# Optimization experiments

Measured on AMD Instinct MI355X. Metric: run time of the kernel, lower is better.

The kernel has to match this reference:

```python
import jax, jax.numpy as jnp
import numpy as np

# ---- config (mirrors the repo-level globals) ----
B, N = 8, 1024                 # batch, points per cloud
SHAPE_SIZE = 256               # per-point shape-code width
HEAD = 8                       # point_size + 1 - shape_size passthrough channels
SC_HID = 256                   # shape_code_encoder_hidden_dims = [256]
SC_OUT = 128                   # shape_code_encoder_output_size
E = 16                         # num_categories
INTER = HEAD + SC_OUT          # 136
ENC_DIMS = [INTER, 256, 512]   # encoder_hidden_dims
LATENT = 1024                  # latent_size
DEC_DIMS = [LATENT, 1024, 2048]
MAX_PTS, PSI = 1024, 7         # max_num_points, point_size_intermediate
DEC_OUT = (PSI + 1) * MAX_PTS  # 8192


def setup_inputs() -> dict:
    key = jax.random.key(0)
    ks = jax.random.split(key, 20)
    s = 0.02
    inp = {
        'x': jax.random.normal(ks[0], (B, HEAD + SHAPE_SIZE, N), jnp.float32),
        'cats': jax.random.randint(ks[1], (B, N), 0, E),
        # per-category shape encoders: Linear(256->256) ReLU Linear(256->128)
        'W1': jax.random.normal(ks[2], (E, SHAPE_SIZE, SC_HID), jnp.float32) * s,
        'b1': jnp.zeros((E, SC_HID), jnp.float32),
        'W2': jax.random.normal(ks[3], (E, SC_HID, SC_OUT), jnp.float32) * s,
        'b2': jnp.zeros((E, SC_OUT), jnp.float32),
        # pointwise Conv1d stack 136->256->512->1024 (weights [out,in])
        'Wc1': jax.random.normal(ks[4], (ENC_DIMS[1], ENC_DIMS[0]), jnp.float32) * s,
        'bc1': jnp.zeros((ENC_DIMS[1],), jnp.float32),
        'Wc2': jax.random.normal(ks[5], (ENC_DIMS[2], ENC_DIMS[1]), jnp.float32) * s,
        'bc2': jnp.zeros((ENC_DIMS[2],), jnp.float32),
        'Wc3': jax.random.normal(ks[6], (LATENT, ENC_DIMS[2]), jnp.float32) * s,
        'bc3': jnp.zeros((LATENT,), jnp.float32),
        # decoder MLP 1024->1024->2048->8192 (weights [in,out])
        'Wd1': jax.random.normal(ks[7], (DEC_DIMS[0], DEC_DIMS[1]), jnp.float32) * s,
        'bd1': jnp.zeros((DEC_DIMS[1],), jnp.float32),
        'Wd2': jax.random.normal(ks[8], (DEC_DIMS[1], DEC_DIMS[2]), jnp.float32) * s,
        'bd2': jnp.zeros((DEC_DIMS[2],), jnp.float32),
        'Wd3': jax.random.normal(ks[9], (DEC_DIMS[2], DEC_OUT), jnp.float32) * s,
        'bd3': jnp.zeros((DEC_OUT,), jnp.float32),
    }
    return inp


def reference(x, cats, W1, b1, W2, b2, Wc1, bc1, Wc2, bc2, Wc3, bc3,
              Wd1, bd1, Wd2, bd2, Wd3, bd3):
    # ---- encoder: category-routed per-point shape MLP ----
    sf = jnp.swapaxes(x[:, -SHAPE_SIZE:, :], 1, 2)      # [B, N, 256]
    mask = jax.nn.one_hot(cats, E, dtype=x.dtype)       # [B, N, E]
    routed = jnp.zeros((B, N, SC_OUT), x.dtype)
    for e in range(E):  # fixed small expert loop; avoids [B,N,E,hid] blowup
        h = jax.nn.relu(sf @ W1[e] + b1[e])             # [B, N, 256]
        o = h @ W2[e] + b2[e]                           # [B, N, 128]
        routed = routed + mask[..., e:e + 1] * o
    xi = jnp.concatenate([x[:, :HEAD, :], jnp.swapaxes(routed, 1, 2)], axis=1)  # [B,136,N]
    # ---- pointwise conv stack + max pool ----
    h = jax.nn.relu(jnp.einsum('oc,bcn->bon', Wc1, xi) + bc1[:, None])
    h = jax.nn.relu(jnp.einsum('oc,bcn->bon', Wc2, h) + bc2[:, None])
    h = jnp.einsum('oc,bcn->bon', Wc3, h) + bc3[:, None]  # [B, 1024, N]
    latent = jnp.max(h, axis=2)                            # [B, 1024]
    # ---- decoder MLP ----
    d = jax.nn.relu(latent @ Wd1 + bd1)
    d = jax.nn.relu(d @ Wd2 + bd2)
    out = (d @ Wd3 + bd3).reshape(B, MAX_PTS, PSI + 1)     # [B, 1024, 8]
    return out, latent
```

## Files before the change

### kernel.cpp

```cpp
#include <hip/hip_runtime.h>
#include <math.h>

#define BB 8
#define NN 1024
#define HEADC 8
#define SS 256
#define SCO 128
#define NE 16
#define C1 256
#define C2 512
#define C3 1024
#define NPTS (BB*NN)
#define XCH (HEADC+SS)
#define K1P 192
#define BK 64

typedef unsigned short ushortT;
typedef __attribute__((ext_vector_type(8))) short bf16x8;
typedef __attribute__((ext_vector_type(4))) float f32x4;

#define OB_XTB   0ull
#define OB_HB    4325376ull
#define OB_H2    0ull
#define OB_XI    8519680ull
#define OB_H1    11665408ull
#define OB_WT1   15859712ull
#define OB_WT2   15958016ull
#define OB_WT3   16220160ull
#define OB_W1T   17268736ull
#define OB_W2T   19365888ull
#define OB_PMAX  20414464ull
#define OB_LAT   20676608ull
#define OB_D1    20709376ull
#define OB_D2    20742144ull
#define OB_DPART 20807680ull
#define OB_IDX   25001984ull
#define OB_OFFS  25034752ull

__device__ __forceinline__ ushortT f2b(float f) {
  unsigned u = __float_as_uint(f);
  return (ushortT)((u + 0x7FFFu + ((u >> 16) & 1u)) >> 16);
}

__global__ __launch_bounds__(256) void k_prep_x(
    const float* __restrict__ x, ushortT* __restrict__ xTb, ushortT* __restrict__ xi) {
  __shared__ float t[32][33];
  int b = blockIdx.z;
  int n0 = blockIdx.x * 32, c0 = blockIdx.y * 32;
  int tx = threadIdx.x & 31, ty = threadIdx.x >> 5;
  const float* s = x + (size_t)b * XCH * NN;
  for (int yy = ty; yy < 32; yy += 8) {
    int c = c0 + yy;
    if (c < XCH) t[yy][tx] = s[(size_t)c * NN + n0 + tx];
  }
  __syncthreads();
  for (int yy = ty; yy < 32; yy += 8) {
    int n = n0 + yy, c = c0 + tx;
    if (c < XCH) {
      ushortT v = f2b(t[tx][yy]);
      xTb[(size_t)(b * NN + n) * XCH + c] = v;
      if (c < HEADC) xi[(size_t)(b * NN + n) * K1P + c] = v;
    }
  }
}

#define CW_S1 (256*192)
#define CW_S2 (512*256)
#define CW_S3 (1024*512)
__global__ __launch_bounds__(256) void k_cvt_weights(
    const float* __restrict__ Wc1, const float* __restrict__ Wc2,
    const float* __restrict__ Wc3, ushortT* __restrict__ w1,
    ushortT* __restrict__ w2, ushortT* __restrict__ w3) {
  int i = blockIdx.x * 256 + threadIdx.x;
  if (i < CW_S1) {
    int r = i / K1P, c = i - r * K1P;
    w1[i] = (c < 136) ? f2b(Wc1[(size_t)r * 136 + c]) : (ushortT)0;
  } else if (i < CW_S1 + CW_S2) {
    int k = i - CW_S1;
    w2[k] = f2b(Wc2[k]);
  } else if (i < CW_S1 + CW_S2 + CW_S3) {
    int k = i - CW_S1 - CW_S2;
    w3[k] = f2b(Wc3[k]);
  }
}

__global__ __launch_bounds__(256) void k_transpose_w12(
    const float* __restrict__ W1, const float* __restrict__ W2,
    ushortT* __restrict__ W1tb, ushortT* __restrict__ W2tb) {
  __shared__ float t[32][33];
  int z = blockIdx.z;
  const float* s;
  ushortT* d;
  int C;
  if (z < 16) { s = W1 + (size_t)z * 65536; d = W1tb + (size_t)z * 65536; C = 256; }
  else {
    if (blockIdx.x >= 4) return;
    s = W2 + (size_t)(z - 16) * 32768; d = W2tb + (size_t)(z - 16) * 32768; C = 128;
  }
  const int R = 256;
  int r0 = blockIdx.y * 32, c0 = blockIdx.x * 32;
  int tx = threadIdx.x & 31, ty = threadIdx.x >> 5;
  for (int yy = ty; yy < 32; yy += 8) {
    int r = r0 + yy, c = c0 + tx;
    if (c < C) t[yy][tx] = s[(size_t)r * C + c];
  }
  __syncthreads();
  for (int yy = ty; yy < 32; yy += 8) {
    int c = c0 + yy, r = r0 + tx;
    if (c < C) d[(size_t)c * R + r] = f2b(t[tx][yy]);
  }
}

__global__ __launch_bounds__(1024) void k_bucket(
    const int* __restrict__ cats, int* __restrict__ idx, int* __restrict__ offs) {
  __shared__ int cnt[NE];
  __shared__ int base[NE + 1];
  __shared__ int cur[NE];
  int tid = threadIdx.x;
  if (tid < NE) cnt[tid] = 0;
  __syncthreads();
  for (int p = tid; p < NPTS; p += 1024) atomicAdd(&cnt[cats[p]], 1);
  __syncthreads();
  if (tid == 0) {
    int s = 0;
    for (int e = 0; e < NE; ++e) { base[e] = s; cur[e] = s; s += cnt[e]; }
    base[NE] = s;
  }
  __syncthreads();
  for (int p = tid; p < NPTS; p += 1024) {
    int pos = atomicAdd(&cur[cats[p]], 1);
    idx[pos] = p;
  }
  if (tid <= NE) offs[tid] = base[tid];
}

template<int MODE>
__global__ __launch_bounds__(256) void k_gemm(
    const ushortT* __restrict__ A, int lda,
    const ushortT* __restrict__ Bt, int ldb,
    const float* __restrict__ bias,
    ushortT* __restrict__ Cb, int ldc,
    float* __restrict__ pmaxOut,
    const int* __restrict__ idx, const int* __restrict__ offsp,
    int K, int relu) {
  __shared__ ushortT As[128 * BK];
  __shared__ ushortT Bs[128 * BK];
  __shared__ int pts[128];
  __shared__ float smax[2][128];
  int tid = threadIdx.x;
  int wave = tid >> 6, lane = tid & 63;
  int wm = wave >> 1, wn = wave & 1;
  int g = lane >> 4, lr = lane & 15;
  int n0 = blockIdx.x * 128;
  int m0 = 0, nr = 128, bucket0 = 0;

  if constexpr (MODE == 2 || MODE == 3) {
    int e = blockIdx.y, t = blockIdx.z;
    int s0 = offsp[e];
    int cnt = offsp[e + 1] - s0;
    int p0 = t * 128;
    if (p0 >= cnt) return;
    nr = min(128, cnt - p0);
    bucket0 = s0 + p0;
    Bt += (size_t)e * ((MODE == 2) ? 256 * 256 : 128 * 256);
    bias += e * ((MODE == 2) ? 256 : 128);
    if (tid < 128) pts[tid] = (tid < nr) ? idx[bucket0 + tid] : 0;
  } else {
    m0 = blockIdx.y * 128;
  }

  f32x4 acc[4][4];
#pragma unroll
  for (int mi = 0; mi < 4; ++mi)
#pragma unroll
    for (int nj = 0; nj < 4; ++nj) acc[mi][nj] = (f32x4)(0.f);

  int nkt = K / BK;
  for (int kt = 0; kt < nkt; ++kt) {
    int k0 = kt * BK;
    __syncthreads();
#pragma unroll
    for (int i = 0; i < 4; ++i) {
      int c = tid + i * 256;
      int row = c >> 3, slot = c & 7;
      int ss = slot ^ (row & 7);
      uint4 v;
      if constexpr (MODE == 2) {
        if (row < nr) v = *(const uint4*)(A + (size_t)pts[row] * lda + 8 + k0 + slot * 8);
        else { v.x = v.y = v.z = v.w = 0u; }
      } else if constexpr (MODE == 3) {
        if (row < nr) v = *(const uint4*)(A + (size_t)(bucket0 + row) * lda + k0 + slot * 8);
        else { v.x = v.y = v.z = v.w = 0u; }
      } else {
        v = *(const uint4*)(A + (size_t)(m0 + row) * lda + k0 + slot * 8);
      }
      *(uint4*)(As + row * BK + ss * 8) = v;
      uint4 w = *(const uint4*)(Bt + (size_t)(n0 + row) * ldb + k0 + slot * 8);
      *(uint4*)(Bs + row * BK + ss * 8) = w;
    }
    __syncthreads();
#pragma unroll
    for (int kk = 0; kk < 2; ++kk) {
      bf16x8 av[4], bv[4];
#pragma unroll
      for (int mi = 0; mi < 4; ++mi) {
        int row = wm * 64 + mi * 16 + lr;
        int slot = (kk * 4 + g) ^ (row & 7);
        av[mi] = *(const bf16x8*)(As + row * BK + slot * 8);
      }
#pragma unroll
      for (int nj = 0; nj < 4; ++nj) {
        int row = wn * 64 + nj * 16 + lr;
        int slot = (kk * 4 + g) ^ (row & 7);
        bv[nj] = *(const bf16x8*)(Bs + row * BK + slot * 8);
      }
#pragma unroll
      for (int mi = 0; mi < 4; ++mi)
#pragma unroll
        for (int nj = 0; nj < 4; ++nj)
          acc[mi][nj] = __builtin_amdgcn_mfma_f32_16x16x32_bf16(av[mi], bv[nj], acc[mi][nj], 0, 0, 0);
    }
  }

  if constexpr (MODE == 1) {
#pragma unroll
    for (int nj = 0; nj < 4; ++nj) {
      float m = -INFINITY;
#pragma unroll
      for (int mi = 0; mi < 4; ++mi)
#pragma unroll
        for (int r = 0; r < 4; ++r) m = fmaxf(m, acc[mi][nj][r]);
      m = fmaxf(m, __shfl_xor(m, 16));
      m = fmaxf(m, __shfl_xor(m, 32));
      if (lane < 16) smax[wm][wn * 64 + nj * 16 + lr] = m;
    }
    __syncthreads();
    if (tid < 128) {
      float m = fmaxf(smax[0][tid], smax[1][tid]);
      pmaxOut[(size_t)blockIdx.y * C3 + n0 + tid] = m + bias[n0 + tid];
    }
  } else {
#pragma unroll
    for (int mi = 0; mi < 4; ++mi)
#pragma unroll
      for (int nj = 0; nj < 4; ++nj)
#pragma unroll
        for (int r = 0; r < 4; ++r) {
          int lrow = wm * 64 + mi * 16 + g * 4 + r;
          int col = n0 + wn * 64 + nj * 16 + lr;
          float v = acc[mi][nj][r] + bias[col];
          if (relu) v = fmaxf(v, 0.f);
          ushortT b = f2b(v);
          if constexpr (MODE == 0) {
            Cb[(size_t)(m0 + lrow) * ldc + col] = b;
          } else if constexpr (MODE == 2) {
            if (lrow < nr) Cb[(size_t)(bucket0 + lrow) * ldc + col] = b;
          } else {
            if (lrow < nr) Cb[(size_t)pts[lrow] * ldc + 8 + col] = b;
          }
        }
  }
}

__global__ __launch_bounds__(256) void k_latmax(
    const float* __restrict__ pmax, float* __restrict__ lat, float* __restrict__ outLat) {
  int id4 = blockIdx.x * 256 + threadIdx.x;
  int b = id4 >> 8, o4 = id4 & 255;
  f32x4 m = (f32x4)(-INFINITY);
  for (int t = 0; t < 8; ++t) {
    f32x4 v = *(const f32x4*)(pmax + (size_t)((b << 3) + t) * C3 + o4 * 4);
#pragma unroll
    for (int r = 0; r < 4; ++r) m[r] = fmaxf(m[r], v[r]);
  }
  *(f32x4*)(lat + (size_t)id4 * 4) = m;
  *(f32x4*)(outLat + (size_t)id4 * 4) = m;
}

__global__ __launch_bounds__(256) void k_dec_part(
    const float* __restrict__ A, const float* __restrict__ W,
    float* __restrict__ part, int K, int N, int chunkLog) {
  __shared__ float a[8 * 128];
  int chunk = 1 << chunkLog;
  int i0 = blockIdx.y << chunkLog;
  int tid = threadIdx.x;
  for (int idx = tid; idx < (8 << chunkLog); idx += blockDim.x) {
    int r = idx >> chunkLog, i = idx & (chunk - 1);
    a[idx] = A[(size_t)r * K + i0 + i];
  }
  __syncthreads();
  int col = (blockIdx.x * blockDim.x + tid) * 4;
  f32x4 acc[8];
#pragma unroll
  for (int r = 0; r < 8; ++r) acc[r] = (f32x4)(0.f);
  const float* wp = W + (size_t)i0 * N + col;
#pragma unroll 2
  for (int k = 0; k < chunk; k += 4) {
    f32x4 w0 = *(const f32x4*)(wp + (size_t)(k + 0) * N);
    f32x4 w1 = *(const f32x4*)(wp + (size_t)(k + 1) * N);
    f32x4 w2 = *(const f32x4*)(wp + (size_t)(k + 2) * N);
    f32x4 w3 = *(const f32x4*)(wp + (size_t)(k + 3) * N);
#pragma unroll
    for (int r = 0; r < 8; ++r) {
      const float* ar = &a[(r << chunkLog) + k];
      acc[r] += ar[0] * w0 + ar[1] * w1 + ar[2] * w2 + ar[3] * w3;
    }
  }
  float* pp = part + (size_t)(blockIdx.y * 8) * N + col;
#pragma unroll
  for (int r = 0; r < 8; ++r) *(f32x4*)(pp + (size_t)r * N) = acc[r];
}

__global__ __launch_bounds__(256) void k_reduce4(
    const float* __restrict__ part, const float* __restrict__ bias,
    float* __restrict__ out, int N, int KC, int doRelu) {
  int o4 = blockIdx.x * 256 + threadIdx.x;
  int col4 = o4 & ((N >> 2) - 1);
  f32x4 s = ((const f32x4*)bias)[col4];
  const f32x4* p4 = (const f32x4*)part;
  for (int kc = 0; kc < KC; ++kc)
    s += p4[(size_t)kc * 2 * N + o4];
  if (doRelu) {
#pragma unroll
    for (int r = 0; r < 4; ++r) s[r] = fmaxf(s[r], 0.f);
  }
  ((f32x4*)out)[o4] = s;
}

extern "C" void kernel_launch(void* const* d_in, const int* in_sizes, int n_in,
                              void* d_out, int out_size, void* d_ws, size_t ws_size,
                              hipStream_t stream) {
  const float* x    = (const float*)d_in[0];
  const int*   cats = (const int*)d_in[1];
  const float* W1   = (const float*)d_in[2];
  const float* b1   = (const float*)d_in[3];
  const float* W2   = (const float*)d_in[4];
  const float* b2   = (const float*)d_in[5];
  const float* Wc1  = (const float*)d_in[6];
  const float* bc1  = (const float*)d_in[7];
  const float* Wc2  = (const float*)d_in[8];
  const float* bc2  = (const float*)d_in[9];
  const float* Wc3  = (const float*)d_in[10];
  const float* bc3  = (const float*)d_in[11];
  const float* Wd1  = (const float*)d_in[12];
  const float* bd1  = (const float*)d_in[13];
  const float* Wd2  = (const float*)d_in[14];
  const float* bd2  = (const float*)d_in[15];
  const float* Wd3  = (const float*)d_in[16];
  const float* bd3  = (const float*)d_in[17];
  float* out = (float*)d_out;

  char* wsb = (char*)d_ws;
  ushortT* xTb  = (ushortT*)(wsb + OB_XTB);
  ushortT* hB   = (ushortT*)(wsb + OB_HB);
  ushortT* h2   = (ushortT*)(wsb + OB_H2);
  ushortT* xi   = (ushortT*)(wsb + OB_XI);
  ushortT* h1   = (ushortT*)(wsb + OB_H1);
  ushortT* Wt1b = (ushortT*)(wsb + OB_WT1);
  ushortT* Wt2b = (ushortT*)(wsb + OB_WT2);
  ushortT* Wt3b = (ushortT*)(wsb + OB_WT3);
  ushortT* W1tb = (ushortT*)(wsb + OB_W1T);
  ushortT* W2tb = (ushortT*)(wsb + OB_W2T);
  float* pmax   = (float*)(wsb + OB_PMAX);
  float* lat    = (float*)(wsb + OB_LAT);
  float* d1w    = (float*)(wsb + OB_D1);
  float* d2w    = (float*)(wsb + OB_D2);
  float* dpart  = (float*)(wsb + OB_DPART);
  int*   idx    = (int*)(wsb + OB_IDX);
  int*   offs   = (int*)(wsb + OB_OFFS);

  k_prep_x<<<dim3(32, 9, BB), 256, 0, stream>>>(x, xTb, xi);
  k_cvt_weights<<<(CW_S1 + CW_S2 + CW_S3 + 255) / 256, 256, 0, stream>>>(
      Wc1, Wc2, Wc3, Wt1b, Wt2b, Wt3b);
  k_transpose_w12<<<dim3(8, 8, 32), 256, 0, stream>>>(W1, W2, W1tb, W2tb);

  k_bucket<<<1, 1024, 0, stream>>>(cats, idx, offs);
  k_gemm<2><<<dim3(2, NE, 8), 256, 0, stream>>>(xTb, XCH, W1tb, 256, b1, hB, 256,
                                                nullptr, idx, offs, 256, 1);
  k_gemm<3><<<dim3(1, NE, 8), 256, 0, stream>>>(hB, 256, W2tb, 256, b2, xi, K1P,
                                                nullptr, idx, offs, 256, 0);

  k_gemm<0><<<dim3(2, 64), 256, 0, stream>>>(xi, K1P, Wt1b, K1P, bc1, h1, 256,
                                             nullptr, nullptr, nullptr, K1P, 1);
  k_gemm<0><<<dim3(4, 64), 256, 0, stream>>>(h1, 256, Wt2b, 256, bc2, h2, 512,
                                             nullptr, nullptr, nullptr, 256, 1);
  k_gemm<1><<<dim3(8, 64), 256, 0, stream>>>(h2, 512, Wt3b, 512, bc3, nullptr, 0,
                                             pmax, nullptr, nullptr, 512, 0);
  k_latmax<<<8, 256, 0, stream>>>(pmax, lat, out + 65536);

  k_dec_part<<<dim3(4, 32), 64, 0, stream>>>(lat, Wd1, dpart, 1024, 1024, 5);
  k_reduce4<<<8, 256, 0, stream>>>(dpart, bd1, d1w, 1024, 32, 1);
  k_dec_part<<<dim3(8, 32), 64, 0, stream>>>(d1w, Wd2, dpart, 1024, 2048, 5);
  k_reduce4<<<16, 256, 0, stream>>>(dpart, bd2, d2w, 2048, 32, 1);
  k_dec_part<<<dim3(8, 16), 256, 0, stream>>>(d2w, Wd3, dpart, 2048, 8192, 7);
  k_reduce4<<<64, 256, 0, stream>>>(dpart, bd3, out, 8192, 16, 0);
  (void)in_sizes; (void)n_in; (void)out_size; (void)ws_size;
}
```

Measured before the change: 306.6 us.

## Merge prep kernels into one launch and fuse decoder split-K reductions into consumers

```diff
diff --git a/kernel.cpp b/kernel.cpp
--- a/kernel.cpp
+++ b/kernel.cpp
@@ -19,119 +19,119 @@
 typedef __attribute__((ext_vector_type(8))) short bf16x8;
 typedef __attribute__((ext_vector_type(4))) float f32x4;
 
-#define OB_XTB   0ull
-#define OB_HB    4325376ull
-#define OB_H2    0ull
-#define OB_XI    8519680ull
-#define OB_H1    11665408ull
-#define OB_WT1   15859712ull
-#define OB_WT2   15958016ull
-#define OB_WT3   16220160ull
-#define OB_W1T   17268736ull
-#define OB_W2T   19365888ull
-#define OB_PMAX  20414464ull
-#define OB_LAT   20676608ull
-#define OB_D1    20709376ull
-#define OB_D2    20742144ull
-#define OB_DPART 20807680ull
-#define OB_IDX   25001984ull
-#define OB_OFFS  25034752ull
+#define OB_XTB    0ull
+#define OB_HB     4325376ull
+#define OB_H2     0ull
+#define OB_XI     8519680ull
+#define OB_H1     11665408ull
+#define OB_WT1    15859712ull
+#define OB_WT2    15958016ull
+#define OB_WT3    16220160ull
+#define OB_W1T    17268736ull
+#define OB_W2T    19365888ull
+#define OB_PMAX   20414464ull
+#define OB_LAT    20676608ull
+#define OB_DPARTA 20807680ull
+#define OB_DPARTB 22904832ull
+#define OB_DPARTC 25001984ull
+#define OB_IDX    33390592ull
+#define OB_OFFS   33423360ull
 
 __device__ __forceinline__ ushortT f2b(float f) {
   unsigned u = __float_as_uint(f);
   return (ushortT)((u + 0x7FFFu + ((u >> 16) & 1u)) >> 16);
 }
 
-__global__ __launch_bounds__(256) void k_prep_x(
-    const float* __restrict__ x, ushortT* __restrict__ xTb, ushortT* __restrict__ xi) {
-  __shared__ float t[32][33];
-  int b = blockIdx.z;
-  int n0 = blockIdx.x * 32, c0 = blockIdx.y * 32;
-  int tx = threadIdx.x & 31, ty = threadIdx.x >> 5;
-  const float* s = x + (size_t)b * XCH * NN;
-  for (int yy = ty; yy < 32; yy += 8) {
-    int c = c0 + yy;
-    if (c < XCH) t[yy][tx] = s[(size_t)c * NN + n0 + tx];
-  }
-  __syncthreads();
-  for (int yy = ty; yy < 32; yy += 8) {
-    int n = n0 + yy, c = c0 + tx;
-    if (c < XCH) {
-      ushortT v = f2b(t[tx][yy]);
-      xTb[(size_t)(b * NN + n) * XCH + c] = v;
-      if (c < HEADC) xi[(size_t)(b * NN + n) * K1P + c] = v;
-    }
-  }
-}
-
 #define CW_S1 (256*192)
 #define CW_S2 (512*256)
 #define CW_S3 (1024*512)
-__global__ __launch_bounds__(256) void k_cvt_weights(
+#define PREP_P1 2304
+#define PREP_P2 5056
+#define PREP_P3 7104
+#define PREP_GRID 7105
+
+__global__ __launch_bounds__(256) void k_prep_all(
+    const float* __restrict__ x, ushortT* __restrict__ xTb, ushortT* __restrict__ xi,
     const float* __restrict__ Wc1, const float* __restrict__ Wc2,
-    const float* __restrict__ Wc3, ushortT* __restrict__ w1,
-    ushortT* __restrict__ w2, ushortT* __restrict__ w3) {
-  int i = blockIdx.x * 256 + threadIdx.x;
-  if (i < CW_S1) {
-    int r = i / K1P, c = i - r * K1P;
-    w1[i] = (c < 136) ? f2b(Wc1[(size_t)r * 136 + c]) : (ushortT)0;
-  } else if (i < CW_S1 + CW_S2) {
-    int k = i - CW_S1;
-    w2[k] = f2b(Wc2[k]);
-  } else if (i < CW_S1 + CW_S2 + CW_S3) {
-    int k = i - CW_S1 - CW_S2;
-    w3[k] = f2b(Wc3[k]);
-  }
-}
-
-__global__ __launch_bounds__(256) void k_transpose_w12(
+    const float* __restrict__ Wc3, ushortT* __restrict__ w1c,
+    ushortT* __restrict__ w2c, ushortT* __restrict__ w3c,
     const float* __restrict__ W1, const float* __restrict__ W2,
-    ushortT* __restrict__ W1tb, ushortT* __restrict__ W2tb) {
+    ushortT* __restrict__ W1tb, ushortT* __restrict__ W2tb,
+    const int* __restrict__ cats, int* __restrict__ idx, int* __restrict__ offs) {
   __shared__ float t[32][33];
-  int z = blockIdx.z;
-  const float* s;
-  ushortT* d;
-  int C;
-  if (z < 16) { s = W1 + (size_t)z * 65536; d = W1tb + (size_t)z * 65536; C = 256; }
-  else {
-    if (blockIdx.x >= 4) return;
-    s = W2 + (size_t)(z - 16) * 32768; d = W2tb + (size_t)(z - 16) * 32768; C = 128;
-  }
-  const int R = 256;
-  int r0 = blockIdx.y * 32, c0 = blockIdx.x * 32;
-  int tx = threadIdx.x & 31, ty = threadIdx.x >> 5;
-  for (int yy = ty; yy < 32; yy += 8) {
-    int r = r0 + yy, c = c0 + tx;
-    if (c < C) t[yy][tx] = s[(size_t)r * C + c];
-  }
-  __syncthreads();
-  for (int yy = ty; yy < 32; yy += 8) {
-    int c = c0 + yy, r = r0 + tx;
-    if (c < C) d[(size_t)c * R + r] = f2b(t[tx][yy]);
-  }
-}
-
-__global__ __launch_bounds__(1024) void k_bucket(
-    const int* __restrict__ cats, int* __restrict__ idx, int* __restrict__ offs) {
-  __shared__ int cnt[NE];
-  __shared__ int base[NE + 1];
-  __shared__ int cur[NE];
+  __shared__ int cnt[NE], base[NE + 1], cur[NE];
+  int bid = blockIdx.x;
   int tid = threadIdx.x;
-  if (tid < NE) cnt[tid] = 0;
-  __syncthreads();
-  for (int p = tid; p < NPTS; p += 1024) atomicAdd(&cnt[cats[p]], 1);
-  __syncthreads();
-  if (tid == 0) {
-    int s = 0;
-    for (int e = 0; e < NE; ++e) { base[e] = s; cur[e] = s; s += cnt[e]; }
-    base[NE] = s;
-  }
-  __syncthreads();
-  for (int p = tid; p < NPTS; p += 1024) {
-    int pos = atomicAdd(&cur[cats[p]], 1);
-    idx[pos] = p;
-  }
-  if (tid <= NE) offs[tid] = base[tid];
+
+  if (bid < PREP_P1) {
+    int bx = bid & 31, by = (bid >> 5) % 9, bz = bid / 288;
+    int n0 = bx * 32, c0 = by * 32;
+    int tx = tid & 31, ty = tid >> 5;
+    const float* s = x + (size_t)bz * XCH * NN;
+    for (int yy = ty; yy < 32; yy += 8) {
+      int c = c0 + yy;
+      if (c < XCH) t[yy][tx] = s[(size_t)c * NN + n0 + tx];
+    }
+    __syncthreads();
+    for (int yy = ty; yy < 32; yy += 8) {
+      int n = n0 + yy, c = c0 + tx;
+      if (c < XCH) {
+        ushortT v = f2b(t[tx][yy]);
+        xTb[(size_t)(bz * NN + n) * XCH + c] = v;
+        if (c < HEADC) xi[(size_t)(bz * NN + n) * K1P + c] = v;
+      }
+    }
+  } else if (bid < PREP_P2) {
+    int i = (bid - PREP_P1) * 256 + tid;
+    if (i < CW_S1) {
+      int r = i / K1P, c = i - r * K1P;
+      w1c[i] = (c < 136) ? f2b(Wc1[(size_t)r * 136 + c]) : (ushortT)0;
+    } else if (i < CW_S1 + CW_S2) {
+      int k = i - CW_S1;
+      w2c[k] = f2b(Wc2[k]);
+    } else if (i < CW_S1 + CW_S2 + CW_S3) {
+      int k = i - CW_S1 - CW_S2;
+      w3c[k] = f2b(Wc3[k]);
+    }
+  } else if (bid < PREP_P3) {
+    int tt = bid - PREP_P2;
+    int z = tt >> 6, ry = (tt >> 3) & 7, cx = tt & 7;
+    const float* s;
+    ushortT* d;
+    int C;
+    if (z < 16) { s = W1 + (size_t)z * 65536; d = W1tb + (size_t)z * 65536; C = 256; }
+    else {
+      if (cx >= 4) return;
+      s = W2 + (size_t)(z - 16) * 32768; d = W2tb + (size_t)(z - 16) * 32768; C = 128;
+    }
+    int r0 = ry * 32, c0 = cx * 32;
+    int tx = tid & 31, ty = tid >> 5;
+    for (int yy = ty; yy < 32; yy += 8) {
+      int r = r0 + yy, c = c0 + tx;
+      if (c < C) t[yy][tx] = s[(size_t)r * C + c];
+    }
+    __syncthreads();
+    for (int yy = ty; yy < 32; yy += 8) {
+      int c = c0 + yy, r = r0 + tx;
+      if (c < C) d[(size_t)c * 256 + r] = f2b(t[tx][yy]);
+    }
+  } else {
+    if (tid < NE) cnt[tid] = 0;
+    __syncthreads();
+    for (int p = tid; p < NPTS; p += 256) atomicAdd(&cnt[cats[p]], 1);
+    __syncthreads();
+    if (tid == 0) {
+      int s = 0;
+      for (int e = 0; e < NE; ++e) { base[e] = s; cur[e] = s; s += cnt[e]; }
+      base[NE] = s;
+    }
+    __syncthreads();
+    for (int p = tid; p < NPTS; p += 256) {
+      int pos = atomicAdd(&cur[cats[p]], 1);
+      idx[pos] = p;
+    }
+    if (tid <= NE) offs[tid] = base[tid];
+  }
 }
 
 template<int MODE>
@@ -276,34 +276,39 @@
   *(f32x4*)(outLat + (size_t)id4 * 4) = m;
 }
 
-__global__ __launch_bounds__(256) void k_dec_part(
-    const float* __restrict__ A, const float* __restrict__ W,
-    float* __restrict__ part, int K, int N, int chunkLog) {
-  __shared__ float a[8 * 128];
-  int chunk = 1 << chunkLog;
-  int i0 = blockIdx.y << chunkLog;
+template<int MODE, int CHUNKLOG, int T, int KCIN>
+__global__ __launch_bounds__(T, 1) void k_dec(
+    const float* __restrict__ Asrc, const float* __restrict__ biasIn,
+    const float* __restrict__ W, float* __restrict__ part, int K, int N) {
+  constexpr int CHUNK = 1 << CHUNKLOG;
+  __shared__ float a[8 << CHUNKLOG];
+  int i0 = blockIdx.y << CHUNKLOG;
   int tid = threadIdx.x;
-  for (int idx = tid; idx < (8 << chunkLog); idx += blockDim.x) {
-    int r = idx >> chunkLog, i = idx & (chunk - 1);
-    a[idx] = A[(size_t)r * K + i0 + i];
+  for (int idx = tid; idx < (8 << CHUNKLOG); idx += T) {
+    int r = idx >> CHUNKLOG, i = idx & (CHUNK - 1);
+    float v;
+    if constexpr (MODE == 0) {
+      v = Asrc[(size_t)r * K + i0 + i];
+    } else {
+      v = biasIn[i0 + i];
+#pragma unroll
+      for (int kc = 0; kc < KCIN; ++kc)
+        v += Asrc[((size_t)kc * 8 + r) * K + i0 + i];
+      v = fmaxf(v, 0.f);
+    }
+    a[idx] = v;
   }
   __syncthreads();
-  int col = (blockIdx.x * blockDim.x + tid) * 4;
+  int col = (blockIdx.x * T + tid) * 4;
   f32x4 acc[8];
 #pragma unroll
   for (int r = 0; r < 8; ++r) acc[r] = (f32x4)(0.f);
   const float* wp = W + (size_t)i0 * N + col;
-#pragma unroll 2
-  for (int k = 0; k < chunk; k += 4) {
-    f32x4 w0 = *(const f32x4*)(wp + (size_t)(k + 0) * N);
-    f32x4 w1 = *(const f32x4*)(wp + (size_t)(k + 1) * N);
-    f32x4 w2 = *(const f32x4*)(wp + (size_t)(k + 2) * N);
-    f32x4 w3 = *(const f32x4*)(wp + (size_t)(k + 3) * N);
-#pragma unroll
-    for (int r = 0; r < 8; ++r) {
-      const float* ar = &a[(r << chunkLog) + k];
-      acc[r] += ar[0] * w0 + ar[1] * w1 + ar[2] * w2 + ar[3] * w3;
-    }
+#pragma unroll 16
+  for (int k = 0; k < CHUNK; ++k) {
+    f32x4 w = *(const f32x4*)(wp + (size_t)k * N);
+#pragma unroll
+    for (int r = 0; r < 8; ++r) acc[r] += a[(r << CHUNKLOG) + k] * w;
   }
   float* pp = part + (size_t)(blockIdx.y * 8) * N + col;
 #pragma unroll
@@ -312,17 +317,14 @@
 
 __global__ __launch_bounds__(256) void k_reduce4(
     const float* __restrict__ part, const float* __restrict__ bias,
-    float* __restrict__ out, int N, int KC, int doRelu) {
+    float* __restrict__ out, int N, int KC) {
   int o4 = blockIdx.x * 256 + threadIdx.x;
   int col4 = o4 & ((N >> 2) - 1);
   f32x4 s = ((const f32x4*)bias)[col4];
   const f32x4* p4 = (const f32x4*)part;
+#pragma unroll 8
   for (int kc = 0; kc < KC; ++kc)
     s += p4[(size_t)kc * 2 * N + o4];
-  if (doRelu) {
-#pragma unroll
-    for (int r = 0; r < 4; ++r) s[r] = fmaxf(s[r], 0.f);
-  }
   ((f32x4*)out)[o4] = s;
 }
 
@@ -362,18 +364,16 @@
   ushortT* W2tb = (ushortT*)(wsb + OB_W2T);
   float* pmax   = (float*)(wsb + OB_PMAX);
   float* lat    = (float*)(wsb + OB_LAT);
-  float* d1w    = (float*)(wsb + OB_D1);
-  float* d2w    = (float*)(wsb + OB_D2);
-  float* dpart  = (float*)(wsb + OB_DPART);
+  float* dpA    = (float*)(wsb + OB_DPARTA);
+  float* dpB    = (float*)(wsb + OB_DPARTB);
+  float* dpC    = (float*)(wsb + OB_DPARTC);
   int*   idx    = (int*)(wsb + OB_IDX);
   int*   offs   = (int*)(wsb + OB_OFFS);
 
-  k_prep_x<<<dim3(32, 9, BB), 256, 0, stream>>>(x, xTb, xi);
-  k_cvt_weights<<<(CW_S1 + CW_S2 + CW_S3 + 255) / 256, 256, 0, stream>>>(
-      Wc1, Wc2, Wc3, Wt1b, Wt2b, Wt3b);
-  k_transpose_w12<<<dim3(8, 8, 32), 256, 0, stream>>>(W1, W2, W1tb, W2tb);
-
-  k_bucket<<<1, 1024, 0, stream>>>(cats, idx, offs);
+  k_prep_all<<<PREP_GRID, 256, 0, stream>>>(
+      x, xTb, xi, Wc1, Wc2, Wc3, Wt1b, Wt2b, Wt3b, W1, W2, W1tb, W2tb,
+      cats, idx, offs);
+
   k_gemm<2><<<dim3(2, NE, 8), 256, 0, stream>>>(xTb, XCH, W1tb, 256, b1, hB, 256,
                                                 nullptr, idx, offs, 256, 1);
   k_gemm<3><<<dim3(1, NE, 8), 256, 0, stream>>>(hB, 256, W2tb, 256, b2, xi, K1P,
@@ -387,11 +387,9 @@
                                              pmax, nullptr, nullptr, 512, 0);
   k_latmax<<<8, 256, 0, stream>>>(pmax, lat, out + 65536);
 
-  k_dec_part<<<dim3(4, 32), 64, 0, stream>>>(lat, Wd1, dpart, 1024, 1024, 5);
-  k_reduce4<<<8, 256, 0, stream>>>(dpart, bd1, d1w, 1024, 32, 1);
-  k_dec_part<<<dim3(8, 32), 64, 0, stream>>>(d1w, Wd2, dpart, 1024, 2048, 5);
-  k_reduce4<<<16, 256, 0, stream>>>(dpart, bd2, d2w, 2048, 32, 1);
-  k_dec_part<<<dim3(8, 16), 256, 0, stream>>>(d2w, Wd3, dpart, 2048, 8192, 7);
-  k_reduce4<<<64, 256, 0, stream>>>(dpart, bd3, out, 8192, 16, 0);
+  k_dec<0, 4, 64, 0><<<dim3(4, 64), 64, 0, stream>>>(lat, nullptr, Wd1, dpA, 1024, 1024);
+  k_dec<1, 5, 64, 64><<<dim3(8, 32), 64, 0, stream>>>(dpA, bd1, Wd2, dpB, 1024, 2048);
+  k_dec<1, 6, 256, 32><<<dim3(8, 32), 256, 0, stream>>>(dpB, bd2, Wd3, dpC, 2048, 8192);
+  k_reduce4<<<64, 256, 0, stream>>>(dpC, bd3, out, 8192, 32);
   (void)in_sizes; (void)n_in; (void)out_size; (void)ws_size;
 }
```

Result: no change. 307.7 us (+0.4%).
